# Optimization experiments

Measured on AMD Instinct MI355X. Metric: run time of the kernel, lower is better.

## Reference

```python
import jax, jax.numpy as jnp
import numpy as np

THRESHOLD = 8.0
BN_EPS = 1e-5


def setup_inputs() -> dict:
    key = jax.random.key(0)
    k1, k2 = jax.random.split(key)
    B, C, H, W = 2, 128, 64, 64
    x = jax.random.normal(k1, (B, C, H, W), dtype=jnp.float32)
    W_fc = jax.random.normal(k2, (C, C), dtype=jnp.float32) * (1.0 / np.sqrt(C))
    b_fc = jnp.zeros((C,), dtype=jnp.float32)
    gamma = jnp.ones((C,), dtype=jnp.float32)
    beta = jnp.zeros((C,), dtype=jnp.float32)
    return {"x": x, "W_fc": W_fc, "b_fc": b_fc, "gamma": gamma, "beta": beta}


def _mean_agg(X, path):
    # X: [B,N,C], path: [B,N,N] (col->row). out = rownorm(path) @ X
    out = jnp.matmul(path, X)
    s = jnp.sum(path, axis=2, keepdims=True)  # [B,N,1]
    norm = jnp.where(s > 0, 1.0 / s, 0.0)     # inf -> 0 as in torch code
    return norm * out


def reference(x, W_fc, b_fc, gamma, beta):
    b, c, h, w = x.shape
    N = h * w
    # [B,N,C] token features
    xf = jnp.transpose(x.reshape(b, c, N), (0, 2, 1))
    # pairwise euclidean distance (cdist, p=2)
    sq = jnp.sum(xf * xf, axis=-1)  # [B,N]
    d2 = sq[:, :, None] + sq[:, None, :] - 2.0 * jnp.einsum('bnc,bmc->bnm', xf, xf)
    dist = jnp.sqrt(jnp.maximum(d2, 0.0))
    Hg = (dist < THRESHOLD).astype(xf.dtype)  # [B,N,N] hypergraph incidence
    # HyperGraphConv: y = fc(x); E = mean(H^T @ y); out = mean(H @ E); res = y + out
    y = jnp.einsum('bnc,dc->bnd', xf, W_fc) + b_fc
    E = _mean_agg(y, jnp.swapaxes(Hg, 1, 2))
    x_out = _mean_agg(E, Hg)
    xe = y + x_out  # [B,N,C]
    # back to [B,C,H,W]
    xo = jnp.transpose(xe, (0, 2, 1)).reshape(b, c, h, w)
    # BatchNorm2d (training mode: batch stats over B,H,W) + SiLU
    mean = jnp.mean(xo, axis=(0, 2, 3), keepdims=True)
    var = jnp.var(xo, axis=(0, 2, 3), keepdims=True)
    xn = (xo - mean) * jax.lax.rsqrt(var + BN_EPS)
    xn = gamma[None, :, None, None] * xn + beta[None, :, None, None]
    return xn * jax.nn.sigmoid(xn)
```

## Files before the change

### kernel.cpp

```cpp
#include <hip/hip_runtime.h>

typedef unsigned short ushort_t;
typedef unsigned int   uint32;
typedef unsigned long long u64;
typedef __bf16 bf16_t;
typedef bf16_t bf16x8 __attribute__((ext_vector_type(8)));
typedef float  f32x4  __attribute__((ext_vector_type(4)));

#define N_TOK 4096
#define C_DIM 128
#define NTOT  8192
#define THRESH2 64.0f

#define XF_OFF  (0u)
#define YF_OFF  (2u<<20)
#define XE_OFF  (10u<<20)
#define SQ_OFF  (14u<<20)
#define BN_OFF  ((14u<<20) + 32768u)
#define HB_OFF  (16u<<20)
#define WS_NEED ((size_t)(24u<<20))

__device__ __forceinline__ ushort_t f2b(float f){
    uint32 u = __float_as_uint(f);
    u += 0x7fffu + ((u>>16)&1u);
    return (ushort_t)(u>>16);
}
__device__ __forceinline__ u64 shfl_u64(u64 v, int src){
    uint32 lo = (uint32)v, hi = (uint32)(v>>32);
    lo = __shfl(lo, src); hi = __shfl(hi, src);
    return ((u64)hi<<32)|lo;
}
__device__ __forceinline__ u64 shfl_xor_u64(u64 v, int m){
    uint32 lo = (uint32)v, hi = (uint32)(v>>32);
    lo = __shfl_xor(lo, m); hi = __shfl_xor(hi, m);
    return ((u64)hi<<32)|lo;
}
__device__ __forceinline__ int wave_popc_reduce(u64 w){
    int cnt = __builtin_popcountll(w);
    cnt += __shfl_xor(cnt, 1);
    cnt += __shfl_xor(cnt, 2);
    cnt += __shfl_xor(cnt, 4);
    cnt += __shfl_xor(cnt, 8);
    cnt += __shfl_xor(cnt, 16);
    cnt += __shfl_xor(cnt, 32);
    return cnt;
}

__global__ __launch_bounds__(256) void k_fc(const float* __restrict__ x,
                                            const float* __restrict__ W,
                                            const float* __restrict__ bfc,
                                            ushort_t* __restrict__ Xf,
                                            float* __restrict__ Yf,
                                            float* __restrict__ sq,
                                            float* __restrict__ bnp){
    __shared__ ushort_t Xs[64*136];
    __shared__ ushort_t Ws[64*136];
    int tid = threadIdx.x;
    int t0 = blockIdx.x * 64;
    int dh = blockIdx.y;
    int b  = t0 >> 12;
    int n0 = t0 & 4095;
    if (blockIdx.x == 0 && dh == 0){
        #pragma unroll
        for (int k=0;k<8;k++) bnp[tid + 256*k] = 0.f;
    }
    const float* xb = x + (size_t)b * C_DIM * N_TOK + n0;
    #pragma unroll
    for (int k=0;k<8;k++){
        int idx = tid + 256*k;
        int c = idx >> 4, n4 = (idx & 15)*4;
        float4 v = *(const float4*)(xb + (size_t)c*N_TOK + n4);
        Xs[(n4+0)*136 + c] = f2b(v.x);
        Xs[(n4+1)*136 + c] = f2b(v.y);
        Xs[(n4+2)*136 + c] = f2b(v.z);
        Xs[(n4+3)*136 + c] = f2b(v.w);
    }
    const float* Wb = W + (size_t)dh*64*C_DIM;
    #pragma unroll
    for (int k=0;k<8;k++){
        int idx = tid + 256*k;
        int d = idx >> 5, c4 = (idx & 31)*4;
        float4 v = *(const float4*)(Wb + d*C_DIM + c4);
        uint2 u;
        u.x = (uint32)f2b(v.x) | ((uint32)f2b(v.y)<<16);
        u.y = (uint32)f2b(v.z) | ((uint32)f2b(v.w)<<16);
        *(uint2*)(&Ws[d*136 + c4]) = u;
    }
    __syncthreads();
    #pragma unroll
    for (int k=0;k<2;k++){
        int idx = tid + 256*(k + 2*dh);
        int row = idx >> 4, c8 = (idx & 15)*8;
        uint4 o = *(const uint4*)(&Xs[row*136 + c8]);
        *(uint4*)(Xf + (size_t)(t0 + row)*C_DIM + c8) = o;
    }
    if (dh == 0){
        int tok = tid >> 2, p = tid & 3;
        const ushort_t* xr = &Xs[tok*136 + p*32];
        float sacc = 0.f;
        #pragma unroll
        for (int i=0;i<16;i++){
            uint32 u = *(const uint32*)(&xr[i*2]);
            float v0 = __uint_as_float(u<<16);
            float v1 = __uint_as_float(u & 0xffff0000u);
            sacc = fmaf(v0, v0, sacc);
            sacc = fmaf(v1, v1, sacc);
        }
        sacc += __shfl_xor(sacc, 1);
        sacc += __shfl_xor(sacc, 2);
        if (p == 0) sq[t0 + tok] = sacc;
    }
    int wv = tid >> 6, lane = tid & 63;
    int qd = lane >> 4, m = lane & 15;
    f32x4 acc[4] = {{0,0,0,0},{0,0,0,0},{0,0,0,0},{0,0,0,0}};
    #pragma unroll
    for (int kc=0;kc<4;kc++){
        bf16x8 af = *(const bf16x8*)(&Xs[(wv*16 + m)*136 + kc*32 + qd*8]);
        #pragma unroll
        for (int ct=0;ct<4;ct++){
            bf16x8 bfr = *(const bf16x8*)(&Ws[(ct*16+m)*136 + kc*32 + qd*8]);
            acc[ct] = __builtin_amdgcn_mfma_f32_16x16x32_bf16(af, bfr, acc[ct], 0, 0, 0);
        }
    }
    int row = t0 + wv*16 + qd*4;
    #pragma unroll
    for (int ct=0;ct<4;ct++){
        int d = dh*64 + ct*16 + m;
        float bias = bfc[d];
        #pragma unroll
        for (int r=0;r<4;r++)
            Yf[(size_t)(row + r)*C_DIM + d] = acc[ct][r] + bias;
    }
}

__global__ __launch_bounds__(256) void k_gram64(const ushort_t* __restrict__ Xf,
                                                const float* __restrict__ sq,
                                                u64* __restrict__ Hb){
    __shared__ ushort_t Al[64*136];
    __shared__ ushort_t Bl[64*136];
    __shared__ u64 rowW[64];
    __shared__ u64 part[256];
    int tid = threadIdx.x;
    int L = blockIdx.x, bb = blockIdx.y;
    int bi = (int)((129.0f - sqrtf(16641.0f - 8.0f*(float)L)) * 0.5f);
    while (bi > 0 && bi*(129-bi)/2 > L) --bi;
    while ((bi+1)*(129-(bi+1))/2 <= L) ++bi;
    int bj = bi + (L - bi*(129-bi)/2);
    int i0 = bi*64, j0 = bj*64;
    const ushort_t* XfA = Xf + (size_t)(bb*N_TOK + i0)*C_DIM;
    const ushort_t* XfB = Xf + (size_t)(bb*N_TOK + j0)*C_DIM;
    #pragma unroll
    for (int k=0;k<4;k++){
        int q = tid + 256*k;
        int row = q >> 4, cp = (q & 15)*8;
        *(uint4*)(&Al[row*136 + cp]) = *(const uint4*)(XfA + row*C_DIM + cp);
        *(uint4*)(&Bl[row*136 + cp]) = *(const uint4*)(XfB + row*C_DIM + cp);
    }
    __syncthreads();
    int wv = tid >> 6, lane = tid & 63;
    int qd = lane >> 4, m = lane & 15;
    f32x4 acc[4] = {{0,0,0,0},{0,0,0,0},{0,0,0,0},{0,0,0,0}};
    #pragma unroll
    for (int kc=0;kc<4;kc++){
        bf16x8 a0 = *(const bf16x8*)(&Al[(wv*16 + m)*136 + kc*32 + qd*8]);
        #pragma unroll
        for (int ct=0;ct<4;ct++){
            bf16x8 bfr = *(const bf16x8*)(&Bl[(ct*16+m)*136 + kc*32 + qd*8]);
            acc[ct] = __builtin_amdgcn_mfma_f32_16x16x32_bf16(a0, bfr, acc[ct], 0, 0, 0);
        }
    }
    float sqj[4];
    #pragma unroll
    for (int ct=0;ct<4;ct++) sqj[ct] = sq[bb*N_TOK + j0 + ct*16 + m];
    int lr = wv*16 + qd*4;
    int ib = i0 + lr;
    float sqi[4];
    #pragma unroll
    for (int r=0;r<4;r++) sqi[r] = sq[bb*N_TOK + ib + r];
    #pragma unroll
    for (int r=0;r<4;r++){
        u64 bits = 0;
        #pragma unroll
        for (int ct=0;ct<4;ct++){
            float d2 = sqi[r] + sqj[ct] - 2.0f*acc[ct][r];
            if (d2 < THRESH2) bits |= (u64)1 << (ct*16 + m);
        }
        bits |= shfl_xor_u64(bits, 1);
        bits |= shfl_xor_u64(bits, 2);
        bits |= shfl_xor_u64(bits, 4);
        bits |= shfl_xor_u64(bits, 8);
        if (m == 0){
            Hb[(size_t)(bb*N_TOK + ib + r)*64 + bj] = bits;
            rowW[lr + r] = bits;
        }
    }
    __syncthreads();
    if (bi != bj){
        int jj = tid & 63, q = tid >> 6;
        u64 p = 0;
        int ibase = q*16;
        #pragma unroll
        for (int ii=0; ii<16; ii++)
            p |= ((rowW[ibase + ii] >> jj) & 1ull) << (ibase + ii);
        part[tid] = p;
        __syncthreads();
        if (tid < 64){
            u64 wt = part[tid] | part[tid+64] | part[tid+128] | part[tid+192];
            Hb[(size_t)(bb*N_TOK + j0 + tid)*64 + bi] = wt;
        }
    }
}

__global__ __launch_bounds__(256) void k_agg2(const u64* __restrict__ Hb,
                                              const float* __restrict__ Yf,
                                              float* __restrict__ Xe,
                                              float* __restrict__ bnp){
    __shared__ float r1[4][128];
    __shared__ float r2[4][128];
    int tid = threadIdx.x;
    int wv = tid >> 6, lane = tid & 63;
    int row = blockIdx.x * 4 + wv;
    int b = row >> 12;
    const float* Vb = Yf + (size_t)b*N_TOK*C_DIM;
    u64 myw = Hb[(size_t)row*64 + lane];
    int cnt = wave_popc_reduce(myw);
    float nrm_i = (cnt > 0) ? 1.0f/(float)cnt : 0.0f;
    float acc0 = 0.f, acc1 = 0.f;
    u64 nz = __ballot(myw != 0);
    while (nz){
        int wdi = __builtin_ctzll(nz);
        nz &= nz - 1;
        u64 mw = shfl_u64(myw, wdi);
        while (mw){
            int j = wdi*64 + __builtin_ctzll(mw);
            mw &= mw - 1;
            int jrow = (b << 12) + j;
            u64 jw; float nrm_j;
            if (jrow == row){
                jw = myw; nrm_j = nrm_i;
            } else {
                jw = Hb[(size_t)jrow*64 + lane];
                int jc = wave_popc_reduce(jw);
                nrm_j = (jc > 0) ? 1.0f/(float)jc : 0.0f;
            }
            float sub0 = 0.f, sub1 = 0.f;
            u64 jnz = __ballot(jw != 0);
            while (jnz){
                int w2 = __builtin_ctzll(jnz);
                jnz &= jnz - 1;
                u64 m2 = shfl_u64(jw, w2);
                while (m2){
                    int kk = w2*64 + __builtin_ctzll(m2);
                    m2 &= m2 - 1;
                    sub0 += Vb[(size_t)kk*C_DIM + lane];
                    sub1 += Vb[(size_t)kk*C_DIM + lane + 64];
                }
            }
            acc0 += nrm_j * sub0;
            acc1 += nrm_j * sub1;
        }
    }
    size_t o = (size_t)row*C_DIM;
    float xe0 = Yf[o + lane]      + nrm_i*acc0;
    float xe1 = Yf[o + lane + 64] + nrm_i*acc1;
    Xe[o + lane]      = xe0;
    Xe[o + lane + 64] = xe1;
    r1[wv][lane]      = xe0;
    r1[wv][lane + 64] = xe1;
    r2[wv][lane]      = xe0*xe0;
    r2[wv][lane + 64] = xe1*xe1;
    __syncthreads();
    if (tid < 128){
        float s1 = r1[0][tid]+r1[1][tid]+r1[2][tid]+r1[3][tid];
        float s2 = r2[0][tid]+r2[1][tid]+r2[2][tid]+r2[3][tid];
        int prt = blockIdx.x & 7;
        atomicAdd(&bnp[prt*256 + tid],       s1);
        atomicAdd(&bnp[prt*256 + 128 + tid], s2);
    }
}

__global__ __launch_bounds__(256) void k_out(const float* __restrict__ Xe,
                                             const float* __restrict__ bnp,
                                             const float* __restrict__ gamma,
                                             const float* __restrict__ beta,
                                             float* __restrict__ out){
    __shared__ float tile[32][33];
    int tx = threadIdx.x, ty = threadIdx.y;
    int n0 = blockIdx.x*32, c0 = blockIdx.y*32, b = blockIdx.z;
    int c = c0 + tx;
    float s1 = 0.f, s2 = 0.f;
    #pragma unroll
    for (int p=0;p<8;p++){
        s1 += bnp[p*256 + c];
        s2 += bnp[p*256 + 128 + c];
    }
    float inv = 1.0f / (float)NTOT;
    float mean = s1 * inv;
    float var  = s2*inv - mean*mean;
    float scale = gamma[c] * rsqrtf(var + 1e-5f);
    float shift = beta[c] - mean*scale;
    #pragma unroll
    for (int k=0;k<4;k++){
        int nl = ty + 8*k;
        float v = Xe[(size_t)(b*N_TOK + n0 + nl)*C_DIM + c];
        v = scale*v + shift;
        float sg = 1.0f/(1.0f + __expf(-v));
        tile[tx][nl] = v * sg;
    }
    __syncthreads();
    #pragma unroll
    for (int k=0;k<4;k++){
        int cl = ty + 8*k;
        out[(size_t)(b*C_DIM + c0 + cl)*N_TOK + n0 + tx] = tile[cl][tx];
    }
}

extern "C" void kernel_launch(void* const* d_in, const int* in_sizes, int n_in,
                              void* d_out, int out_size, void* d_ws, size_t ws_size,
                              hipStream_t stream){
    if (ws_size < WS_NEED) return;
    const float* x     = (const float*)d_in[0];
    const float* W     = (const float*)d_in[1];
    const float* bfc   = (const float*)d_in[2];
    const float* gamma = (const float*)d_in[3];
    const float* beta  = (const float*)d_in[4];
    char* ws = (char*)d_ws;
    ushort_t* Xf = (ushort_t*)(ws + XF_OFF);
    float*    Yf = (float*)(ws + YF_OFF);
    float*    Xe = (float*)(ws + XE_OFF);
    float*    sqp= (float*)(ws + SQ_OFF);
    float*    bnp= (float*)(ws + BN_OFF);
    u64*      Hb = (u64*)(ws + HB_OFF);
    float*    outp = (float*)d_out;

    k_fc    <<<dim3(128,2),  dim3(256),   0, stream>>>(x, W, bfc, Xf, Yf, sqp, bnp);
    k_gram64<<<dim3(2080,2), dim3(256),   0, stream>>>(Xf, sqp, Hb);
    k_agg2  <<<dim3(2048),   dim3(256),   0, stream>>>(Hb, Yf, Xe, bnp);
    k_out   <<<dim3(128,4,2),dim3(32,8),  0, stream>>>(Xe, bnp, gamma, beta, outp);
}
```

Baseline: 103.3 us.

## Fuse FC and Gram kernels into one launch, recomputing bf16 tokens per tile

Merges the FC projection kernel and the pairwise-distance Gram kernel into one launch. The first 256 blocks compute the FC and the rest build incidence tiles. Gram blocks now read x directly, convert it to bf16, transpose it into LDS and compute squared norms locally, so the Xf and sq intermediates and their dependency barrier go away. The cost is redundant conversion and transposed strided loads of x in every Gram tile, which reads more global data than the compact bf16 Xf did.

```diff
diff --git a/kernel.cpp b/kernel.cpp
--- a/kernel.cpp
+++ b/kernel.cpp
@@ -12,10 +12,8 @@
 #define NTOT  8192
 #define THRESH2 64.0f
 
-#define XF_OFF  (0u)
 #define YF_OFF  (2u<<20)
 #define XE_OFF  (10u<<20)
-#define SQ_OFF  (14u<<20)
 #define BN_OFF  ((14u<<20) + 32768u)
 #define HB_OFF  (16u<<20)
 #define WS_NEED ((size_t)(24u<<20))
@@ -46,167 +44,183 @@
     return cnt;
 }
 
-__global__ __launch_bounds__(256) void k_fc(const float* __restrict__ x,
-                                            const float* __restrict__ W,
-                                            const float* __restrict__ bfc,
-                                            ushort_t* __restrict__ Xf,
-                                            float* __restrict__ Yf,
-                                            float* __restrict__ sq,
-                                            float* __restrict__ bnp){
-    __shared__ ushort_t Xs[64*136];
-    __shared__ ushort_t Ws[64*136];
+union SMem {
+    struct { ushort_t Xs[64*136]; ushort_t Ws[64*136]; } fc;
+    struct { ushort_t Al[64*136]; ushort_t Bl[64*136]; u64 rowW[64]; u64 part[256];
+             float sqA[64]; float sqB[64]; } gr;
+};
+
+__global__ __launch_bounds__(256) void k_fcgram(const float* __restrict__ x,
+                                                const float* __restrict__ W,
+                                                const float* __restrict__ bfc,
+                                                float* __restrict__ Yf,
+                                                float* __restrict__ bnp,
+                                                u64* __restrict__ Hb){
+    __shared__ SMem sm;
     int tid = threadIdx.x;
-    int t0 = blockIdx.x * 64;
-    int dh = blockIdx.y;
-    int b  = t0 >> 12;
-    int n0 = t0 & 4095;
-    if (blockIdx.x == 0 && dh == 0){
-        #pragma unroll
-        for (int k=0;k<8;k++) bnp[tid + 256*k] = 0.f;
-    }
-    const float* xb = x + (size_t)b * C_DIM * N_TOK + n0;
-    #pragma unroll
-    for (int k=0;k<8;k++){
-        int idx = tid + 256*k;
-        int c = idx >> 4, n4 = (idx & 15)*4;
-        float4 v = *(const float4*)(xb + (size_t)c*N_TOK + n4);
-        Xs[(n4+0)*136 + c] = f2b(v.x);
-        Xs[(n4+1)*136 + c] = f2b(v.y);
-        Xs[(n4+2)*136 + c] = f2b(v.z);
-        Xs[(n4+3)*136 + c] = f2b(v.w);
-    }
-    const float* Wb = W + (size_t)dh*64*C_DIM;
-    #pragma unroll
-    for (int k=0;k<8;k++){
-        int idx = tid + 256*k;
-        int d = idx >> 5, c4 = (idx & 31)*4;
-        float4 v = *(const float4*)(Wb + d*C_DIM + c4);
-        uint2 u;
-        u.x = (uint32)f2b(v.x) | ((uint32)f2b(v.y)<<16);
-        u.y = (uint32)f2b(v.z) | ((uint32)f2b(v.w)<<16);
-        *(uint2*)(&Ws[d*136 + c4]) = u;
-    }
-    __syncthreads();
-    #pragma unroll
-    for (int k=0;k<2;k++){
-        int idx = tid + 256*(k + 2*dh);
-        int row = idx >> 4, c8 = (idx & 15)*8;
-        uint4 o = *(const uint4*)(&Xs[row*136 + c8]);
-        *(uint4*)(Xf + (size_t)(t0 + row)*C_DIM + c8) = o;
-    }
-    if (dh == 0){
-        int tok = tid >> 2, p = tid & 3;
-        const ushort_t* xr = &Xs[tok*136 + p*32];
-        float sacc = 0.f;
-        #pragma unroll
-        for (int i=0;i<16;i++){
-            uint32 u = *(const uint32*)(&xr[i*2]);
-            float v0 = __uint_as_float(u<<16);
-            float v1 = __uint_as_float(u & 0xffff0000u);
-            sacc = fmaf(v0, v0, sacc);
-            sacc = fmaf(v1, v1, sacc);
-        }
-        sacc += __shfl_xor(sacc, 1);
-        sacc += __shfl_xor(sacc, 2);
-        if (p == 0) sq[t0 + tok] = sacc;
-    }
-    int wv = tid >> 6, lane = tid & 63;
-    int qd = lane >> 4, m = lane & 15;
-    f32x4 acc[4] = {{0,0,0,0},{0,0,0,0},{0,0,0,0},{0,0,0,0}};
-    #pragma unroll
-    for (int kc=0;kc<4;kc++){
-        bf16x8 af = *(const bf16x8*)(&Xs[(wv*16 + m)*136 + kc*32 + qd*8]);
+    int bid = blockIdx.x;
+
+    if (bid < 256){
+        int t0 = (bid >> 1) * 64;
+        int dh = bid & 1;
+        int b  = t0 >> 12;
+        int n0 = t0 & 4095;
+        if (bid == 0){
+            #pragma unroll
+            for (int k=0;k<8;k++) bnp[tid + 256*k] = 0.f;
+        }
+        const float* xb = x + (size_t)b * C_DIM * N_TOK + n0;
+        #pragma unroll
+        for (int k=0;k<8;k++){
+            int idx = tid + 256*k;
+            int c = idx >> 4, n4 = (idx & 15)*4;
+            float4 v = *(const float4*)(xb + (size_t)c*N_TOK + n4);
+            sm.fc.Xs[(n4+0)*136 + c] = f2b(v.x);
+            sm.fc.Xs[(n4+1)*136 + c] = f2b(v.y);
+            sm.fc.Xs[(n4+2)*136 + c] = f2b(v.z);
+            sm.fc.Xs[(n4+3)*136 + c] = f2b(v.w);
+        }
+        const float* Wb = W + (size_t)dh*64*C_DIM;
+        #pragma unroll
+        for (int k=0;k<8;k++){
+            int idx = tid + 256*k;
+            int d = idx >> 5, c4 = (idx & 31)*4;
+            float4 v = *(const float4*)(Wb + d*C_DIM + c4);
+            uint2 u;
+            u.x = (uint32)f2b(v.x) | ((uint32)f2b(v.y)<<16);
+            u.y = (uint32)f2b(v.z) | ((uint32)f2b(v.w)<<16);
+            *(uint2*)(&sm.fc.Ws[d*136 + c4]) = u;
+        }
+        __syncthreads();
+        int wv = tid >> 6, lane = tid & 63;
+        int qd = lane >> 4, m = lane & 15;
+        f32x4 acc[4] = {{0,0,0,0},{0,0,0,0},{0,0,0,0},{0,0,0,0}};
+        #pragma unroll
+        for (int kc=0;kc<4;kc++){
+            bf16x8 af = *(const bf16x8*)(&sm.fc.Xs[(wv*16 + m)*136 + kc*32 + qd*8]);
+            #pragma unroll
+            for (int ct=0;ct<4;ct++){
+                bf16x8 bfr = *(const bf16x8*)(&sm.fc.Ws[(ct*16+m)*136 + kc*32 + qd*8]);
+                acc[ct] = __builtin_amdgcn_mfma_f32_16x16x32_bf16(af, bfr, acc[ct], 0, 0, 0);
+            }
+        }
+        int row = t0 + wv*16 + qd*4;
         #pragma unroll
         for (int ct=0;ct<4;ct++){
-            bf16x8 bfr = *(const bf16x8*)(&Ws[(ct*16+m)*136 + kc*32 + qd*8]);
-            acc[ct] = __builtin_amdgcn_mfma_f32_16x16x32_bf16(af, bfr, acc[ct], 0, 0, 0);
-        }
-    }
-    int row = t0 + wv*16 + qd*4;
-    #pragma unroll
-    for (int ct=0;ct<4;ct++){
-        int d = dh*64 + ct*16 + m;
-        float bias = bfc[d];
-        #pragma unroll
-        for (int r=0;r<4;r++)
-            Yf[(size_t)(row + r)*C_DIM + d] = acc[ct][r] + bias;
-    }
-}
-
-__global__ __launch_bounds__(256) void k_gram64(const ushort_t* __restrict__ Xf,
-                                                const float* __restrict__ sq,
-                                                u64* __restrict__ Hb){
-    __shared__ ushort_t Al[64*136];
-    __shared__ ushort_t Bl[64*136];
-    __shared__ u64 rowW[64];
-    __shared__ u64 part[256];
-    int tid = threadIdx.x;
-    int L = blockIdx.x, bb = blockIdx.y;
-    int bi = (int)((129.0f - sqrtf(16641.0f - 8.0f*(float)L)) * 0.5f);
-    while (bi > 0 && bi*(129-bi)/2 > L) --bi;
-    while ((bi+1)*(129-(bi+1))/2 <= L) ++bi;
-    int bj = bi + (L - bi*(129-bi)/2);
-    int i0 = bi*64, j0 = bj*64;
-    const ushort_t* XfA = Xf + (size_t)(bb*N_TOK + i0)*C_DIM;
-    const ushort_t* XfB = Xf + (size_t)(bb*N_TOK + j0)*C_DIM;
-    #pragma unroll
-    for (int k=0;k<4;k++){
-        int q = tid + 256*k;
-        int row = q >> 4, cp = (q & 15)*8;
-        *(uint4*)(&Al[row*136 + cp]) = *(const uint4*)(XfA + row*C_DIM + cp);
-        *(uint4*)(&Bl[row*136 + cp]) = *(const uint4*)(XfB + row*C_DIM + cp);
-    }
-    __syncthreads();
-    int wv = tid >> 6, lane = tid & 63;
-    int qd = lane >> 4, m = lane & 15;
-    f32x4 acc[4] = {{0,0,0,0},{0,0,0,0},{0,0,0,0},{0,0,0,0}};
-    #pragma unroll
-    for (int kc=0;kc<4;kc++){
-        bf16x8 a0 = *(const bf16x8*)(&Al[(wv*16 + m)*136 + kc*32 + qd*8]);
-        #pragma unroll
-        for (int ct=0;ct<4;ct++){
-            bf16x8 bfr = *(const bf16x8*)(&Bl[(ct*16+m)*136 + kc*32 + qd*8]);
-            acc[ct] = __builtin_amdgcn_mfma_f32_16x16x32_bf16(a0, bfr, acc[ct], 0, 0, 0);
-        }
-    }
-    float sqj[4];
-    #pragma unroll
-    for (int ct=0;ct<4;ct++) sqj[ct] = sq[bb*N_TOK + j0 + ct*16 + m];
-    int lr = wv*16 + qd*4;
-    int ib = i0 + lr;
-    float sqi[4];
-    #pragma unroll
-    for (int r=0;r<4;r++) sqi[r] = sq[bb*N_TOK + ib + r];
-    #pragma unroll
-    for (int r=0;r<4;r++){
-        u64 bits = 0;
-        #pragma unroll
-        for (int ct=0;ct<4;ct++){
-            float d2 = sqi[r] + sqj[ct] - 2.0f*acc[ct][r];
-            if (d2 < THRESH2) bits |= (u64)1 << (ct*16 + m);
-        }
-        bits |= shfl_xor_u64(bits, 1);
-        bits |= shfl_xor_u64(bits, 2);
-        bits |= shfl_xor_u64(bits, 4);
-        bits |= shfl_xor_u64(bits, 8);
-        if (m == 0){
-            Hb[(size_t)(bb*N_TOK + ib + r)*64 + bj] = bits;
-            rowW[lr + r] = bits;
-        }
-    }
-    __syncthreads();
-    if (bi != bj){
-        int jj = tid & 63, q = tid >> 6;
-        u64 p = 0;
-        int ibase = q*16;
-        #pragma unroll
-        for (int ii=0; ii<16; ii++)
-            p |= ((rowW[ibase + ii] >> jj) & 1ull) << (ibase + ii);
-        part[tid] = p;
+            int d = dh*64 + ct*16 + m;
+            float bias = bfc[d];
+            #pragma unroll
+            for (int r=0;r<4;r++)
+                Yf[(size_t)(row + r)*C_DIM + d] = acc[ct][r] + bias;
+        }
+    } else {
+        int t = bid - 256;
+        int bb = (t >= 2080) ? 1 : 0;
+        int L = t - bb*2080;
+        int bi = (int)((129.0f - sqrtf(16641.0f - 8.0f*(float)L)) * 0.5f);
+        while (bi > 0 && bi*(129-bi)/2 > L) --bi;
+        while ((bi+1)*(129-(bi+1))/2 <= L) ++bi;
+        int bj = bi + (L - bi*(129-bi)/2);
+        int i0 = bi*64, j0 = bj*64;
+        const float* xb = x + (size_t)bb * C_DIM * N_TOK;
+        #pragma unroll
+        for (int k=0;k<8;k++){
+            int idx = tid + 256*k;
+            int c = idx >> 4, n4 = (idx & 15)*4;
+            const float* xc = xb + (size_t)c*N_TOK;
+            float4 va = *(const float4*)(xc + i0 + n4);
+            sm.gr.Al[(n4+0)*136 + c] = f2b(va.x);
+            sm.gr.Al[(n4+1)*136 + c] = f2b(va.y);
+            sm.gr.Al[(n4+2)*136 + c] = f2b(va.z);
+            sm.gr.Al[(n4+3)*136 + c] = f2b(va.w);
+            float4 vb = *(const float4*)(xc + j0 + n4);
+            sm.gr.Bl[(n4+0)*136 + c] = f2b(vb.x);
+            sm.gr.Bl[(n4+1)*136 + c] = f2b(vb.y);
+            sm.gr.Bl[(n4+2)*136 + c] = f2b(vb.z);
+            sm.gr.Bl[(n4+3)*136 + c] = f2b(vb.w);
+        }
         __syncthreads();
-        if (tid < 64){
-            u64 wt = part[tid] | part[tid+64] | part[tid+128] | part[tid+192];
-            Hb[(size_t)(bb*N_TOK + j0 + tid)*64 + bi] = wt;
+        {
+            int tok = tid >> 2, p = tid & 3;
+            const ushort_t* xr = &sm.gr.Al[tok*136 + p*32];
+            float sacc = 0.f;
+            #pragma unroll
+            for (int i=0;i<16;i++){
+                uint32 u = *(const uint32*)(&xr[i*2]);
+                float v0 = __uint_as_float(u<<16);
+                float v1 = __uint_as_float(u & 0xffff0000u);
+                sacc = fmaf(v0, v0, sacc);
+                sacc = fmaf(v1, v1, sacc);
+            }
+            sacc += __shfl_xor(sacc, 1);
+            sacc += __shfl_xor(sacc, 2);
+            if (p == 0) sm.gr.sqA[tok] = sacc;
+            xr = &sm.gr.Bl[tok*136 + p*32];
+            sacc = 0.f;
+            #pragma unroll
+            for (int i=0;i<16;i++){
+                uint32 u = *(const uint32*)(&xr[i*2]);
+                float v0 = __uint_as_float(u<<16);
+                float v1 = __uint_as_float(u & 0xffff0000u);
+                sacc = fmaf(v0, v0, sacc);
+                sacc = fmaf(v1, v1, sacc);
+            }
+            sacc += __shfl_xor(sacc, 1);
+            sacc += __shfl_xor(sacc, 2);
+            if (p == 0) sm.gr.sqB[tok] = sacc;
+        }
+        int wv = tid >> 6, lane = tid & 63;
+        int qd = lane >> 4, m = lane & 15;
+        f32x4 acc[4] = {{0,0,0,0},{0,0,0,0},{0,0,0,0},{0,0,0,0}};
+        #pragma unroll
+        for (int kc=0;kc<4;kc++){
+            bf16x8 a0 = *(const bf16x8*)(&sm.gr.Al[(wv*16 + m)*136 + kc*32 + qd*8]);
+            #pragma unroll
+            for (int ct=0;ct<4;ct++){
+                bf16x8 bfr = *(const bf16x8*)(&sm.gr.Bl[(ct*16+m)*136 + kc*32 + qd*8]);
+                acc[ct] = __builtin_amdgcn_mfma_f32_16x16x32_bf16(a0, bfr, acc[ct], 0, 0, 0);
+            }
+        }
+        __syncthreads();
+        float sqj[4];
+        #pragma unroll
+        for (int ct=0;ct<4;ct++) sqj[ct] = sm.gr.sqB[ct*16 + m];
+        int lr = wv*16 + qd*4;
+        int ib = i0 + lr;
+        float sqi[4];
+        #pragma unroll
+        for (int r=0;r<4;r++) sqi[r] = sm.gr.sqA[lr + r];
+        #pragma unroll
+        for (int r=0;r<4;r++){
+            u64 bits = 0;
+            #pragma unroll
+            for (int ct=0;ct<4;ct++){
+                float d2 = sqi[r] + sqj[ct] - 2.0f*acc[ct][r];
+                if (d2 < THRESH2) bits |= (u64)1 << (ct*16 + m);
+            }
+            bits |= shfl_xor_u64(bits, 1);
+            bits |= shfl_xor_u64(bits, 2);
+            bits |= shfl_xor_u64(bits, 4);
+            bits |= shfl_xor_u64(bits, 8);
+            if (m == 0){
+                Hb[(size_t)(bb*N_TOK + ib + r)*64 + bj] = bits;
+                sm.gr.rowW[lr + r] = bits;
+            }
+        }
+        __syncthreads();
+        if (bi != bj){
+            int jj = tid & 63, q = tid >> 6;
+            u64 p = 0;
+            int ibase = q*16;
+            #pragma unroll
+            for (int ii=0; ii<16; ii++)
+                p |= ((sm.gr.rowW[ibase + ii] >> jj) & 1ull) << (ibase + ii);
+            sm.gr.part[tid] = p;
+            __syncthreads();
+            if (tid < 64){
+                u64 wt = sm.gr.part[tid] | sm.gr.part[tid+64] | sm.gr.part[tid+128] | sm.gr.part[tid+192];
+                Hb[(size_t)(bb*N_TOK + j0 + tid)*64 + bi] = wt;
+            }
         }
     }
 }
@@ -325,16 +339,13 @@
     const float* gamma = (const float*)d_in[3];
     const float* beta  = (const float*)d_in[4];
     char* ws = (char*)d_ws;
-    ushort_t* Xf = (ushort_t*)(ws + XF_OFF);
     float*    Yf = (float*)(ws + YF_OFF);
     float*    Xe = (float*)(ws + XE_OFF);
-    float*    sqp= (float*)(ws + SQ_OFF);
     float*    bnp= (float*)(ws + BN_OFF);
     u64*      Hb = (u64*)(ws + HB_OFF);
     float*    outp = (float*)d_out;
 
-    k_fc    <<<dim3(128,2),  dim3(256),   0, stream>>>(x, W, bfc, Xf, Yf, sqp, bnp);
-    k_gram64<<<dim3(2080,2), dim3(256),   0, stream>>>(Xf, sqp, Hb);
+    k_fcgram<<<dim3(4416),   dim3(256),   0, stream>>>(x, W, bfc, Yf, bnp, Hb);
     k_agg2  <<<dim3(2048),   dim3(256),   0, stream>>>(Hb, Yf, Xe, bnp);
     k_out   <<<dim3(128,4,2),dim3(32,8),  0, stream>>>(Xe, bnp, gamma, beta, outp);
 }
```

New measurement: 133.6 us. 29.4% more time.
